# Optimization experiments

Hardware: AMD Instinct MI355X
Metric: run time of the kernel (lower is better)

Reference implementation:

```python
import jax, jax.numpy as jnp
import numpy as np

NUM_STEPS = 5


def setup_inputs() -> dict:
    key = jax.random.key(0)
    ks = jax.random.split(key, 12)
    B, N, H, E, A = 8, 1024, 64, 2, 8
    initial_state = jax.random.normal(ks[0], (B, N, H), dtype=jnp.float32)
    annotation = jax.random.normal(ks[1], (B, N, A), dtype=jnp.float32)
    # sparse-ish positive adjacency, scaled so matmul outputs don't saturate gates
    adj_matrix = jax.random.uniform(ks[2], (B, N, 2 * N * E), dtype=jnp.float32) * 0.01
    s = 0.05
    W_edge = jax.random.normal(ks[3], (H, H * E), dtype=jnp.float32) * s
    b_edge = jax.random.normal(ks[4], (H * E,), dtype=jnp.float32) * s
    W_gate = jax.random.normal(ks[5], (3 * H, H), dtype=jnp.float32) * s
    b_gate = jax.random.normal(ks[6], (H,), dtype=jnp.float32) * s
    W_hid = jax.random.normal(ks[7], (H + A, H), dtype=jnp.float32) * s
    b_hid = jax.random.normal(ks[8], (H,), dtype=jnp.float32) * s
    W_out = jax.random.normal(ks[9], (H, 1), dtype=jnp.float32) * s
    b_out = jax.random.normal(ks[10], (1,), dtype=jnp.float32) * s
    return dict(initial_state=initial_state, annotation=annotation, adj_matrix=adj_matrix,
                W_edge=W_edge, b_edge=b_edge, W_gate=W_gate, b_gate=b_gate,
                W_hid=W_hid, b_hid=b_hid, W_out=W_out, b_out=b_out)


def reference(initial_state, annotation, adj_matrix, W_edge, b_edge,
              W_gate, b_gate, W_hid, b_hid, W_out, b_out):
    B, N, H = initial_state.shape
    E = W_edge.shape[1] // H
    boundary = N * E
    A_in = adj_matrix[:, :, :boundary]   # [B, N, N*E]
    A_out = adj_matrix[:, :, boundary:]  # [B, N, N*E]

    h = initial_state
    for _ in range(NUM_STEPS):
        # Linear(H, H*E) then view/transpose to [B, N*E, H].
        # Original computes incoming_edge and outgoing_edge with the SAME
        # linear on the SAME input -> identical tensors; compute once.
        edge = jnp.einsum('bnh,he->bne', h, W_edge) + b_edge      # [B, N, H*E]
        edge = edge.reshape(B, N, H, E).transpose(0, 3, 1, 2).reshape(B, N * E, H)
        a_in = jnp.matmul(A_in, edge)    # [B, N, H]
        a_out = jnp.matmul(A_out, edge)  # [B, N, H]
        a = jnp.concatenate([a_in, a_out, h], axis=2)             # [B, N, 3H]
        # update and reset use the same gate linear -> equal; compute once.
        z = jax.nn.sigmoid(jnp.einsum('bnk,kh->bnh', a, W_gate) + b_gate)
        a_r = jnp.concatenate([a_in, a_out, z * h], axis=2)
        h_tilde = jnp.tanh(jnp.einsum('bnk,kh->bnh', a_r, W_gate) + b_gate)
        h = (1.0 - z) * h + z * h_tilde

    # task_id not in {18, 19}: node-level output head
    ha = jnp.concatenate([h, annotation], axis=2)                 # [B, N, H+A]
    out = jnp.tanh(jnp.einsum('bnk,kh->bnh', ha, W_hid) + b_hid)  # [B, N, H]
    out = (jnp.einsum('bnh,ho->bno', out, W_out) + b_out).sum(axis=2)  # [B, N]
    return out
```

## Files before the change

kernel.cpp:

```cpp
#include <hip/hip_runtime.h>
#include <math.h>

#define BN    8
#define NN    1024
#define HH    64
#define ADIM  8
#define STEPS 5
#define K2    2048
#define ROWS  (BN*NN)

typedef __attribute__((ext_vector_type(8))) short bf16x8;
typedef __attribute__((ext_vector_type(4))) float f32x4;

__device__ __forceinline__ unsigned short f2bf(float f) {
    unsigned int u = __float_as_uint(f);
    u += 0x7FFF + ((u >> 16) & 1);
    return (unsigned short)(u >> 16);
}
__device__ __forceinline__ float bf2f(unsigned short h) {
    return __uint_as_float(((unsigned int)h) << 16);
}

__global__ __launch_bounds__(256) void conv_adj(
    const float* __restrict__ in, unsigned short* __restrict__ out)
{
    int tid = blockIdx.x * 256 + threadIdx.x;
    #pragma unroll
    for (int i = 0; i < 4; ++i) {
        size_t idx = (size_t)tid + (size_t)i * 2097152;
        float4 v = ((const float4*)in)[idx];
        ushort4 o;
        o.x = f2bf(v.x); o.y = f2bf(v.y); o.z = f2bf(v.z); o.w = f2bf(v.w);
        ((ushort4*)out)[idx] = o;
    }
}

__global__ __launch_bounds__(256) void prep_pack(
    const float* __restrict__ Wg, const float* __restrict__ We,
    unsigned short* __restrict__ wgp, unsigned short* __restrict__ wep)
{
    int t = blockIdx.x * 256 + threadIdx.x;
    if (t < 12288) {
        int k = t >> 6, c = t & 63;
        float v = Wg[t];
        unsigned short hi = f2bf(v);
        unsigned short lo = f2bf(v - bf2f(hi));
        wgp[(size_t)c * 192 + k] = hi;
        wgp[(size_t)(64 + c) * 192 + k] = lo;
    } else if (t < 20480) {
        int u = t - 12288;
        int k = u >> 7, c = u & 127;
        float v = We[u];
        unsigned short hi = f2bf(v);
        unsigned short lo = f2bf(v - bf2f(hi));
        wep[(size_t)c * 64 + k] = hi;
        wep[(size_t)(128 + c) * 64 + k] = lo;
    }
}

__global__ __launch_bounds__(256) void init_kernel(
    const float* __restrict__ init_state,
    const float* __restrict__ We, const float* __restrict__ be,
    float* __restrict__ h_ws, unsigned short* __restrict__ edge_t)
{
    __shared__ float h_lds[4][65];
    int t = threadIdx.x;
    int r = t >> 6, hp = t & 63;
    int row = blockIdx.x * 4 + r;
    float hv = init_state[(size_t)row * 64 + hp];
    h_ws[(size_t)row * 64 + hp] = hv;
    h_lds[r][hp] = hv;
    __syncthreads();
    int b = row >> 10, n = row & 1023;
    #pragma unroll
    for (int e = 0; e < 2; ++e) {
        float acc = be[hp * 2 + e];
        #pragma unroll 8
        for (int c = 0; c < 64; ++c)
            acc += h_lds[r][c] * We[c * 128 + hp * 2 + e];
        edge_t[((size_t)b * 64 + hp) * K2 + e * NN + n] = f2bf(acc);
    }
}

__global__ __launch_bounds__(512) void step_kernel(
    const unsigned short* __restrict__ adjb,
    const unsigned short* __restrict__ ein,
    unsigned short* __restrict__ eout,
    float* __restrict__ h_ws,
    const unsigned short* __restrict__ wgp,
    const unsigned short* __restrict__ wep,
    const float* __restrict__ bg,
    const float* __restrict__ be,
    int do_edge)
{
    __shared__ __attribute__((aligned(16))) unsigned short Bs[2][64][264];
    __shared__ __attribute__((aligned(16))) unsigned short Xhi[32][200];
    __shared__ __attribute__((aligned(16))) unsigned short Xlo[32][200];
    __shared__ __attribute__((aligned(16))) float          hf [32][68];
    __shared__ __attribute__((aligned(16))) unsigned short HNhi[32][72];
    __shared__ __attribute__((aligned(16))) unsigned short HNlo[32][72];

    int t  = threadIdx.x;
    int b  = blockIdx.x >> 5;
    int mt = blockIdx.x & 31;
    int n0 = mt * 32;
    size_t hbase = ((size_t)(b * NN + n0)) * 64;

    {
        int r = t >> 4, cg = (t & 15) * 4;
        float4 v = *(const float4*)(h_ws + hbase + (size_t)r * 64 + cg);
        float vv[4] = {v.x, v.y, v.z, v.w};
        #pragma unroll
        for (int j = 0; j < 4; ++j) {
            float hv = vv[j];
            unsigned short hi = f2bf(hv), lo = f2bf(hv - bf2f(hi));
            Xhi[r][128 + cg + j] = hi;
            Xlo[r][128 + cg + j] = lo;
            hf[r][cg + j] = hv;
        }
    }

    int lane = t & 63, w = t >> 6, l15 = lane & 15, q = lane >> 4;
    int dir = w >> 2, rh = (w >> 1) & 1, kc = w & 1;

    const unsigned short* Abase = adjb
        + ((size_t)(b * NN + n0 + rh * 16 + l15)) * 4096 + dir * K2 + kc * 128;

    int srow[4], scol[4];
    const unsigned short* sptr[4];
    #pragma unroll
    for (int i = 0; i < 4; ++i) {
        int u = i * 512 + t;
        srow[i] = u >> 5; scol[i] = (u & 31) * 8;
        sptr[i] = ein + ((size_t)b * 64 + srow[i]) * K2 + scol[i];
    }
    #pragma unroll
    for (int i = 0; i < 4; ++i)
        *(uint4*)&Bs[0][srow[i]][scol[i]] = *(const uint4*)(sptr[i]);
    __syncthreads();

    f32x4 acc[4];
    #pragma unroll
    for (int ct = 0; ct < 4; ++ct) acc[ct] = (f32x4){0.f, 0.f, 0.f, 0.f};

    bf16x8 af[4];
    #pragma unroll
    for (int ks = 0; ks < 4; ++ks)
        af[ks] = *(const bf16x8*)(Abase + ks * 32 + q * 8);

    #pragma unroll
    for (int c = 0; c < 8; ++c) {
        int buf = c & 1;
        uint4 g[4];
        bf16x8 afn[4];
        if (c < 7) {
            #pragma unroll
            for (int i = 0; i < 4; ++i)
                g[i] = *(const uint4*)(sptr[i] + (c + 1) * 256);
            #pragma unroll
            for (int ks = 0; ks < 4; ++ks)
                afn[ks] = *(const bf16x8*)(Abase + (c + 1) * 256 + ks * 32 + q * 8);
        }
        #pragma unroll
        for (int ks = 0; ks < 4; ++ks) {
            #pragma unroll
            for (int ct = 0; ct < 4; ++ct) {
                bf16x8 bfr = *(const bf16x8*)&Bs[buf][ct * 16 + l15][kc * 128 + ks * 32 + q * 8];
                acc[ct] = __builtin_amdgcn_mfma_f32_16x16x32_bf16(af[ks], bfr, acc[ct], 0, 0, 0);
            }
        }
        if (c < 7) {
            #pragma unroll
            for (int i = 0; i < 4; ++i)
                *(uint4*)&Bs[buf ^ 1][srow[i]][scol[i]] = g[i];
            #pragma unroll
            for (int ks = 0; ks < 4; ++ks) af[ks] = afn[ks];
        }
        __syncthreads();
    }

    float (*red)[16][68] = (float (*)[16][68])(&Bs[0][0][0]);
    int gg = w >> 1;
    if (kc == 1) {
        #pragma unroll
        for (int ct = 0; ct < 4; ++ct)
            #pragma unroll
            for (int i = 0; i < 4; ++i)
                red[gg][q * 4 + i][ct * 16 + l15] = acc[ct][i];
    }
    __syncthreads();
    if (kc == 0) {
        #pragma unroll
        for (int ct = 0; ct < 4; ++ct)
            #pragma unroll
            for (int i = 0; i < 4; ++i) {
                float v = acc[ct][i] + red[gg][q * 4 + i][ct * 16 + l15];
                unsigned short hi = f2bf(v), lo = f2bf(v - bf2f(hi));
                int r  = rh * 16 + q * 4 + i;
                int cc = dir * 64 + ct * 16 + l15;
                Xhi[r][cc] = hi;
                Xlo[r][cc] = lo;
            }
    }
    __syncthreads();

    int mg = w & 1, cg16 = w >> 1;
    int arow = mg * 16 + l15;
    int cc = cg16 * 16 + l15;
    const unsigned short* wcol = wgp + (size_t)cc * 192;
    f32x4 as = (f32x4){0.f, 0.f, 0.f, 0.f}, az;

    #pragma unroll
    for (int ks = 0; ks < 4; ++ks) {
        bf16x8 ah = *(const bf16x8*)&Xhi[arow][ks * 32 + q * 8];
        bf16x8 al = *(const bf16x8*)&Xlo[arow][ks * 32 + q * 8];
        const unsigned short* wb = wcol + ks * 32 + q * 8;
        bf16x8 bh = *(const bf16x8*)wb;
        bf16x8 bl = *(const bf16x8*)(wb + 64 * 192);
        as = __builtin_amdgcn_mfma_f32_16x16x32_bf16(ah, bh, as, 0, 0, 0);
        as = __builtin_amdgcn_mfma_f32_16x16x32_bf16(ah, bl, as, 0, 0, 0);
        as = __builtin_amdgcn_mfma_f32_16x16x32_bf16(al, bh, as, 0, 0, 0);
    }
    az = as;
    #pragma unroll
    for (int ks = 4; ks < 6; ++ks) {
        bf16x8 ah = *(const bf16x8*)&Xhi[arow][ks * 32 + q * 8];
        bf16x8 al = *(const bf16x8*)&Xlo[arow][ks * 32 + q * 8];
        const unsigned short* wb = wcol + ks * 32 + q * 8;
        bf16x8 bh = *(const bf16x8*)wb;
        bf16x8 bl = *(const bf16x8*)(wb + 64 * 192);
        az = __builtin_amdgcn_mfma_f32_16x16x32_bf16(ah, bh, az, 0, 0, 0);
        az = __builtin_amdgcn_mfma_f32_16x16x32_bf16(ah, bl, az, 0, 0, 0);
        az = __builtin_amdgcn_mfma_f32_16x16x32_bf16(al, bh, az, 0, 0, 0);
    }
    __syncthreads();

    float zv[4], hv[4];
    float bgv = bg[cc];
    #pragma unroll
    for (int i = 0; i < 4; ++i) {
        int r = mg * 16 + q * 4 + i;
        float z = 1.f / (1.f + __expf(-(az[i] + bgv)));
        float h = hf[r][cc];
        zv[i] = z; hv[i] = h;
        float zh = z * h;
        unsigned short hi = f2bf(zh), lo = f2bf(zh - bf2f(hi));
        Xhi[r][128 + cc] = hi;
        Xlo[r][128 + cc] = lo;
    }
    __syncthreads();

    #pragma unroll
    for (int ks = 4; ks < 6; ++ks) {
        bf16x8 ah = *(const bf16x8*)&Xhi[arow][ks * 32 + q * 8];
        bf16x8 al = *(const bf16x8*)&Xlo[arow][ks * 32 + q * 8];
        const unsigned short* wb = wcol + ks * 32 + q * 8;
        bf16x8 bh = *(const bf16x8*)wb;
        bf16x8 bl = *(const bf16x8*)(wb + 64 * 192);
        as = __builtin_amdgcn_mfma_f32_16x16x32_bf16(ah, bh, as, 0, 0, 0);
        as = __builtin_amdgcn_mfma_f32_16x16x32_bf16(ah, bl, as, 0, 0, 0);
        as = __builtin_amdgcn_mfma_f32_16x16x32_bf16(al, bh, as, 0, 0, 0);
    }

    #pragma unroll
    for (int i = 0; i < 4; ++i) {
        int r = mg * 16 + q * 4 + i;
        float ht = tanhf(as[i] + bgv);
        float z  = zv[i];
        float hn = (1.f - z) * hv[i] + z * ht;
        h_ws[hbase + (size_t)r * 64 + cc] = hn;
        if (do_edge) {
            unsigned short hi = f2bf(hn), lo = f2bf(hn - bf2f(hi));
            HNhi[r][cc] = hi;
            HNlo[r][cc] = lo;
        }
    }
    if (!do_edge) return;
    __syncthreads();

    int me = w & 1, cb2 = (w >> 1) * 2;
    int erow = me * 16 + l15;
    f32x4 ae[2];
    ae[0] = ae[1] = (f32x4){0.f, 0.f, 0.f, 0.f};
    #pragma unroll
    for (int ks = 0; ks < 2; ++ks) {
        bf16x8 ah = *(const bf16x8*)&HNhi[erow][ks * 32 + q * 8];
        bf16x8 al = *(const bf16x8*)&HNlo[erow][ks * 32 + q * 8];
        #pragma unroll
        for (int p = 0; p < 2; ++p) {
            int ec = (cb2 + p) * 16 + l15;
            const unsigned short* wb = wep + (size_t)ec * 64 + ks * 32 + q * 8;
            bf16x8 bh = *(const bf16x8*)wb;
            bf16x8 bl = *(const bf16x8*)(wb + 128 * 64);
            ae[p] = __builtin_amdgcn_mfma_f32_16x16x32_bf16(ah, bh, ae[p], 0, 0, 0);
            ae[p] = __builtin_amdgcn_mfma_f32_16x16x32_bf16(ah, bl, ae[p], 0, 0, 0);
            ae[p] = __builtin_amdgcn_mfma_f32_16x16x32_bf16(al, bh, ae[p], 0, 0, 0);
        }
    }
    #pragma unroll
    for (int p = 0; p < 2; ++p) {
        int ec = (cb2 + p) * 16 + l15;
        float bev = be[ec];
        int hp2 = ec >> 1, e = ec & 1;
        size_t ebase = ((size_t)b * 64 + hp2) * K2 + (size_t)e * NN
                     + n0 + me * 16 + q * 4;
        ushort4 ev;
        ev.x = f2bf(ae[p][0] + bev);
        ev.y = f2bf(ae[p][1] + bev);
        ev.z = f2bf(ae[p][2] + bev);
        ev.w = f2bf(ae[p][3] + bev);
        *(ushort4*)(eout + ebase) = ev;
    }
}

__global__ __launch_bounds__(256) void head_kernel(
    const float* __restrict__ h_ws, const float* __restrict__ ann,
    const float* __restrict__ Wh, const float* __restrict__ bh,
    const float* __restrict__ Wo, const float* __restrict__ bo,
    float* __restrict__ out)
{
    __shared__ float Wh_l[72 * 64];
    __shared__ float ha[4][72];
    int t = threadIdx.x;
    #pragma unroll
    for (int l = 0; l < 18; ++l) {
        int idx = t + l * 256;
        Wh_l[idx] = Wh[idx];
    }
    int r = t >> 6, hp = t & 63;
    int row = blockIdx.x * 4 + r;
    ha[r][hp] = h_ws[(size_t)row * 64 + hp];
    if (hp < ADIM) ha[r][64 + hp] = ann[(size_t)row * ADIM + hp];
    __syncthreads();

    float acc = bh[hp];
    #pragma unroll 8
    for (int k = 0; k < 72; ++k)
        acc += ha[r][k] * Wh_l[k * 64 + hp];
    float v = tanhf(acc) * Wo[hp];
    #pragma unroll
    for (int o = 32; o; o >>= 1) v += __shfl_down(v, o, 64);
    if (hp == 0) out[row] = v + bo[0];
}

extern "C" void kernel_launch(void* const* d_in, const int* in_sizes, int n_in,
                              void* d_out, int out_size, void* d_ws, size_t ws_size,
                              hipStream_t stream) {
    const float* init_state = (const float*)d_in[0];
    const float* ann = (const float*)d_in[1];
    const float* adj = (const float*)d_in[2];
    const float* We  = (const float*)d_in[3];
    const float* be  = (const float*)d_in[4];
    const float* Wg  = (const float*)d_in[5];
    const float* bg  = (const float*)d_in[6];
    const float* Wh  = (const float*)d_in[7];
    const float* bh  = (const float*)d_in[8];
    const float* Wo  = (const float*)d_in[9];
    const float* bo  = (const float*)d_in[10];
    float* out = (float*)d_out;

    char* wsb = (char*)d_ws;
    unsigned short* adj_bf = (unsigned short*)wsb;
    unsigned short* edge_a = (unsigned short*)(wsb + 67108864);
    unsigned short* edge_b = (unsigned short*)(wsb + 69206016);
    float*          h_ws   = (float*)(wsb + 71303168);
    unsigned short* wgp    = (unsigned short*)(wsb + 73400320);
    unsigned short* wep    = (unsigned short*)(wsb + 73449472);

    conv_adj<<<dim3(8192), dim3(256), 0, stream>>>(adj, adj_bf);
    prep_pack<<<dim3(80), dim3(256), 0, stream>>>(Wg, We, wgp, wep);
    init_kernel<<<dim3(ROWS / 4), dim3(256), 0, stream>>>(init_state, We, be, h_ws, edge_a);
    for (int s = 0; s < STEPS; ++s) {
        const unsigned short* ein = (s & 1) ? edge_b : edge_a;
        unsigned short* eo        = (s & 1) ? edge_a : edge_b;
        step_kernel<<<dim3(256), dim3(512), 0, stream>>>(
            adj_bf, ein, eo, h_ws, wgp, wep, bg, be, (s < STEPS - 1) ? 1 : 0);
    }
    head_kernel<<<dim3(ROWS / 4), dim3(256), 0, stream>>>(h_ws, ann, Wh, bh, Wo, bo, out);
}
```

Measured before the change: 384.1 us.

## Pre-tile adjacency and edge buffers into MFMA fragment layout, drop LDS staging

The bf16 adjacency conversion now writes a tiled layout, and the edge tensor is stored in a matching tiled layout. Each MFMA fragment becomes one contiguous 16-byte load per lane straight from global memory. The step kernel's LDS double-buffered B staging, its barriers and its register prefetch pipeline are replaced by direct global loads in a simple unrolled loop. This removes LDS traffic and synchronisation, but load latency now has to be hidden by the unroll and by occupancy, and each B fragment is re-read from global or L2 by every wave.

```diff
diff --git a/kernel.cpp b/kernel.cpp
--- a/kernel.cpp
+++ b/kernel.cpp
@@ -21,17 +21,24 @@
     return __uint_as_float(((unsigned int)h) << 16);
 }
 
+
 __global__ __launch_bounds__(256) void conv_adj(
     const float* __restrict__ in, unsigned short* __restrict__ out)
 {
     int tid = blockIdx.x * 256 + threadIdx.x;
-    #pragma unroll
-    for (int i = 0; i < 4; ++i) {
-        size_t idx = (size_t)tid + (size_t)i * 2097152;
-        float4 v = ((const float4*)in)[idx];
+    int r   = tid >> 7;
+    int dkb = tid & 127;
+    int b = r >> 10, n = r & 1023;
+    int dir = dkb >> 6, kb = dkb & 63;
+    const float* src = in + ((size_t)r << 12) + (dkb << 5);
+    unsigned short* dst = out
+        + ((((((size_t)b * 2 + dir) * 64 + kb) * 64 + (n >> 4)) << 4) + (n & 15)) * 32;
+    #pragma unroll
+    for (int i = 0; i < 8; ++i) {
+        float4 v = ((const float4*)src)[i];
         ushort4 o;
         o.x = f2bf(v.x); o.y = f2bf(v.y); o.z = f2bf(v.z); o.w = f2bf(v.w);
-        ((ushort4*)out)[idx] = o;
+        ((ushort4*)dst)[i] = o;
     }
 }
 
@@ -58,6 +65,12 @@
     }
 }
 
+__device__ __forceinline__ size_t edge_addr(int b, int h, int k) {
+    int kb = k >> 5, hb = h >> 4;
+    return (((size_t)b * 64 + kb) * 4 + hb) * 512
+         + (size_t)(h & 15) * 32 + (k & 31);
+}
+
 __global__ __launch_bounds__(256) void init_kernel(
     const float* __restrict__ init_state,
     const float* __restrict__ We, const float* __restrict__ be,
@@ -78,12 +91,12 @@
         #pragma unroll 8
         for (int c = 0; c < 64; ++c)
             acc += h_lds[r][c] * We[c * 128 + hp * 2 + e];
-        edge_t[((size_t)b * 64 + hp) * K2 + e * NN + n] = f2bf(acc);
+        edge_t[edge_addr(b, hp, e * NN + n)] = f2bf(acc);
     }
 }
 
 __global__ __launch_bounds__(512) void step_kernel(
-    const unsigned short* __restrict__ adjb,
+    const unsigned short* __restrict__ adjf,
     const unsigned short* __restrict__ ein,
     unsigned short* __restrict__ eout,
     float* __restrict__ h_ws,
@@ -93,12 +106,12 @@
     const float* __restrict__ be,
     int do_edge)
 {
-    __shared__ __attribute__((aligned(16))) unsigned short Bs[2][64][264];
     __shared__ __attribute__((aligned(16))) unsigned short Xhi[32][200];
     __shared__ __attribute__((aligned(16))) unsigned short Xlo[32][200];
     __shared__ __attribute__((aligned(16))) float          hf [32][68];
     __shared__ __attribute__((aligned(16))) unsigned short HNhi[32][72];
     __shared__ __attribute__((aligned(16))) unsigned short HNlo[32][72];
+    __shared__ __attribute__((aligned(16))) float          red[4][16][68];
 
     int t  = threadIdx.x;
     int b  = blockIdx.x >> 5;
@@ -122,64 +135,28 @@
 
     int lane = t & 63, w = t >> 6, l15 = lane & 15, q = lane >> 4;
     int dir = w >> 2, rh = (w >> 1) & 1, kc = w & 1;
-
-    const unsigned short* Abase = adjb
-        + ((size_t)(b * NN + n0 + rh * 16 + l15)) * 4096 + dir * K2 + kc * 128;
-
-    int srow[4], scol[4];
-    const unsigned short* sptr[4];
-    #pragma unroll
-    for (int i = 0; i < 4; ++i) {
-        int u = i * 512 + t;
-        srow[i] = u >> 5; scol[i] = (u & 31) * 8;
-        sptr[i] = ein + ((size_t)b * 64 + srow[i]) * K2 + scol[i];
-    }
-    #pragma unroll
-    for (int i = 0; i < 4; ++i)
-        *(uint4*)&Bs[0][srow[i]][scol[i]] = *(const uint4*)(sptr[i]);
-    __syncthreads();
+    int nb  = mt * 2 + rh;
+    int loff = l15 * 32 + q * 8;
+
+    const unsigned short* Ap = adjf
+        + ((((size_t)(b * 2 + dir) * 64 + kc * 32) * 64 + nb) * 512) + loff;
+    const unsigned short* Bp = ein
+        + (((size_t)b * 64 + kc * 32) * 4) * 512 + loff;
 
     f32x4 acc[4];
     #pragma unroll
     for (int ct = 0; ct < 4; ++ct) acc[ct] = (f32x4){0.f, 0.f, 0.f, 0.f};
 
-    bf16x8 af[4];
-    #pragma unroll
-    for (int ks = 0; ks < 4; ++ks)
-        af[ks] = *(const bf16x8*)(Abase + ks * 32 + q * 8);
-
-    #pragma unroll
-    for (int c = 0; c < 8; ++c) {
-        int buf = c & 1;
-        uint4 g[4];
-        bf16x8 afn[4];
-        if (c < 7) {
-            #pragma unroll
-            for (int i = 0; i < 4; ++i)
-                g[i] = *(const uint4*)(sptr[i] + (c + 1) * 256);
-            #pragma unroll
-            for (int ks = 0; ks < 4; ++ks)
-                afn[ks] = *(const bf16x8*)(Abase + (c + 1) * 256 + ks * 32 + q * 8);
+    #pragma unroll 4
+    for (int kb = 0; kb < 32; ++kb) {
+        bf16x8 af = *(const bf16x8*)(Ap + kb * 32768);
+        #pragma unroll
+        for (int ct = 0; ct < 4; ++ct) {
+            bf16x8 bfr = *(const bf16x8*)(Bp + kb * 2048 + ct * 512);
+            acc[ct] = __builtin_amdgcn_mfma_f32_16x16x32_bf16(af, bfr, acc[ct], 0, 0, 0);
         }
-        #pragma unroll
-        for (int ks = 0; ks < 4; ++ks) {
-            #pragma unroll
-            for (int ct = 0; ct < 4; ++ct) {
-                bf16x8 bfr = *(const bf16x8*)&Bs[buf][ct * 16 + l15][kc * 128 + ks * 32 + q * 8];
-                acc[ct] = __builtin_amdgcn_mfma_f32_16x16x32_bf16(af[ks], bfr, acc[ct], 0, 0, 0);
-            }
-        }
-        if (c < 7) {
-            #pragma unroll
-            for (int i = 0; i < 4; ++i)
-                *(uint4*)&Bs[buf ^ 1][srow[i]][scol[i]] = g[i];
-            #pragma unroll
-            for (int ks = 0; ks < 4; ++ks) af[ks] = afn[ks];
-        }
-        __syncthreads();
-    }
-
-    float (*red)[16][68] = (float (*)[16][68])(&Bs[0][0][0]);
+    }
+
     int gg = w >> 1;
     if (kc == 1) {
         #pragma unroll
@@ -301,15 +278,14 @@
     for (int p = 0; p < 2; ++p) {
         int ec = (cb2 + p) * 16 + l15;
         float bev = be[ec];
-        int hp2 = ec >> 1, e = ec & 1;
-        size_t ebase = ((size_t)b * 64 + hp2) * K2 + (size_t)e * NN
-                     + n0 + me * 16 + q * 4;
+        int h = ec >> 1, e = ec & 1;
+        int k = e * NN + n0 + me * 16 + q * 4;
         ushort4 ev;
         ev.x = f2bf(ae[p][0] + bev);
         ev.y = f2bf(ae[p][1] + bev);
         ev.z = f2bf(ae[p][2] + bev);
         ev.w = f2bf(ae[p][3] + bev);
-        *(ushort4*)(eout + ebase) = ev;
+        *(ushort4*)(eout + edge_addr(b, h, k)) = ev;
     }
 }
 
@@ -360,21 +336,21 @@
     float* out = (float*)d_out;
 
     char* wsb = (char*)d_ws;
-    unsigned short* adj_bf = (unsigned short*)wsb;
+    unsigned short* adj_f  = (unsigned short*)wsb;
     unsigned short* edge_a = (unsigned short*)(wsb + 67108864);
     unsigned short* edge_b = (unsigned short*)(wsb + 69206016);
     float*          h_ws   = (float*)(wsb + 71303168);
     unsigned short* wgp    = (unsigned short*)(wsb + 73400320);
     unsigned short* wep    = (unsigned short*)(wsb + 73449472);
 
-    conv_adj<<<dim3(8192), dim3(256), 0, stream>>>(adj, adj_bf);
+    conv_adj<<<dim3(4096), dim3(256), 0, stream>>>(adj, adj_f);
     prep_pack<<<dim3(80), dim3(256), 0, stream>>>(Wg, We, wgp, wep);
     init_kernel<<<dim3(ROWS / 4), dim3(256), 0, stream>>>(init_state, We, be, h_ws, edge_a);
     for (int s = 0; s < STEPS; ++s) {
         const unsigned short* ein = (s & 1) ? edge_b : edge_a;
         unsigned short* eo        = (s & 1) ? edge_a : edge_b;
         step_kernel<<<dim3(256), dim3(512), 0, stream>>>(
-            adj_bf, ein, eo, h_ws, wgp, wep, bg, be, (s < STEPS - 1) ? 1 : 0);
+            adj_f, ein, eo, h_ws, wgp, wep, bg, be, (s < STEPS - 1) ? 1 : 0);
     }
     head_kernel<<<dim3(ROWS / 4), dim3(256), 0, stream>>>(h_ws, ann, Wh, bh, Wo, bo, out);
 }
```

Result: slower. 429.8 us (+11.9%).

## Fuse all stages into one cooperative persistent kernel with grid syncs

Applied to the files above, without the earlier changes.

Merges adjacency bf16 conversion, weight packing, initial edge projection, the five GGNN steps and the output head into a single cooperative kernel of 256 blocks. Steps are separated by grid.sync, and the hidden state stays in LDS across steps instead of going through global memory. This removes about eight kernel launches and the h round-trips through global memory. In exchange, the large adjacency conversion now runs on only 256 blocks, grid-wide barriers add cost, and the rows each block converts may not match the rows it later reads. The adjacency conversion is followed only by a grid sync, so later reads by other blocks rely on that barrier for ordering.

```diff
diff --git a/kernel.cpp b/kernel.cpp
--- a/kernel.cpp
+++ b/kernel.cpp
@@ -1,5 +1,8 @@
 #include <hip/hip_runtime.h>
+#include <hip/hip_cooperative_groups.h>
 #include <math.h>
+
+namespace cg = cooperative_groups;
 
 #define BN    8
 #define NN    1024
@@ -21,77 +24,20 @@
     return __uint_as_float(((unsigned int)h) << 16);
 }
 
-__global__ __launch_bounds__(256) void conv_adj(
-    const float* __restrict__ in, unsigned short* __restrict__ out)
-{
-    int tid = blockIdx.x * 256 + threadIdx.x;
-    #pragma unroll
-    for (int i = 0; i < 4; ++i) {
-        size_t idx = (size_t)tid + (size_t)i * 2097152;
-        float4 v = ((const float4*)in)[idx];
-        ushort4 o;
-        o.x = f2bf(v.x); o.y = f2bf(v.y); o.z = f2bf(v.z); o.w = f2bf(v.w);
-        ((ushort4*)out)[idx] = o;
-    }
-}
-
-__global__ __launch_bounds__(256) void prep_pack(
-    const float* __restrict__ Wg, const float* __restrict__ We,
-    unsigned short* __restrict__ wgp, unsigned short* __restrict__ wep)
-{
-    int t = blockIdx.x * 256 + threadIdx.x;
-    if (t < 12288) {
-        int k = t >> 6, c = t & 63;
-        float v = Wg[t];
-        unsigned short hi = f2bf(v);
-        unsigned short lo = f2bf(v - bf2f(hi));
-        wgp[(size_t)c * 192 + k] = hi;
-        wgp[(size_t)(64 + c) * 192 + k] = lo;
-    } else if (t < 20480) {
-        int u = t - 12288;
-        int k = u >> 7, c = u & 127;
-        float v = We[u];
-        unsigned short hi = f2bf(v);
-        unsigned short lo = f2bf(v - bf2f(hi));
-        wep[(size_t)c * 64 + k] = hi;
-        wep[(size_t)(128 + c) * 64 + k] = lo;
-    }
-}
-
-__global__ __launch_bounds__(256) void init_kernel(
+__global__ __launch_bounds__(512) void mega(
+    const float* __restrict__ adj,
     const float* __restrict__ init_state,
+    const float* __restrict__ ann,
     const float* __restrict__ We, const float* __restrict__ be,
-    float* __restrict__ h_ws, unsigned short* __restrict__ edge_t)
-{
-    __shared__ float h_lds[4][65];
-    int t = threadIdx.x;
-    int r = t >> 6, hp = t & 63;
-    int row = blockIdx.x * 4 + r;
-    float hv = init_state[(size_t)row * 64 + hp];
-    h_ws[(size_t)row * 64 + hp] = hv;
-    h_lds[r][hp] = hv;
-    __syncthreads();
-    int b = row >> 10, n = row & 1023;
-    #pragma unroll
-    for (int e = 0; e < 2; ++e) {
-        float acc = be[hp * 2 + e];
-        #pragma unroll 8
-        for (int c = 0; c < 64; ++c)
-            acc += h_lds[r][c] * We[c * 128 + hp * 2 + e];
-        edge_t[((size_t)b * 64 + hp) * K2 + e * NN + n] = f2bf(acc);
-    }
-}
-
-__global__ __launch_bounds__(512) void step_kernel(
-    const unsigned short* __restrict__ adjb,
-    const unsigned short* __restrict__ ein,
-    unsigned short* __restrict__ eout,
-    float* __restrict__ h_ws,
-    const unsigned short* __restrict__ wgp,
-    const unsigned short* __restrict__ wep,
-    const float* __restrict__ bg,
-    const float* __restrict__ be,
-    int do_edge)
+    const float* __restrict__ Wg, const float* __restrict__ bg,
+    const float* __restrict__ Wh, const float* __restrict__ bh,
+    const float* __restrict__ Wo, const float* __restrict__ bo,
+    unsigned short* __restrict__ adjb,
+    unsigned short* __restrict__ edge_a,
+    unsigned short* __restrict__ edge_b,
+    unsigned short* __restrict__ wgp,
+    unsigned short* __restrict__ wep,
+    float* __restrict__ out)
 {
     __shared__ __attribute__((aligned(16))) unsigned short Bs[2][64][264];
     __shared__ __attribute__((aligned(16))) unsigned short Xhi[32][200];
@@ -100,6 +46,8 @@
     __shared__ __attribute__((aligned(16))) unsigned short HNhi[32][72];
     __shared__ __attribute__((aligned(16))) unsigned short HNlo[32][72];
 
+    cg::grid_group grid = cg::this_grid();
+
     int t  = threadIdx.x;
     int b  = blockIdx.x >> 5;
     int mt = blockIdx.x & 31;
@@ -107,18 +55,65 @@
     size_t hbase = ((size_t)(b * NN + n0)) * 64;
 
     {
-        int r = t >> 4, cg = (t & 15) * 4;
-        float4 v = *(const float4*)(h_ws + hbase + (size_t)r * 64 + cg);
-        float vv[4] = {v.x, v.y, v.z, v.w};
-        #pragma unroll
-        for (int j = 0; j < 4; ++j) {
-            float hv = vv[j];
-            unsigned short hi = f2bf(hv), lo = f2bf(hv - bf2f(hi));
-            Xhi[r][128 + cg + j] = hi;
-            Xlo[r][128 + cg + j] = lo;
-            hf[r][cg + j] = hv;
-        }
-    }
+        int gtid = blockIdx.x * 512 + t;
+        const float4* src = (const float4*)adj;
+        ushort4* dst = (ushort4*)adjb;
+        #pragma unroll 8
+        for (int i = 0; i < 64; ++i) {
+            size_t idx = (size_t)gtid + (size_t)i * 131072;
+            float4 v = src[idx];
+            ushort4 o;
+            o.x = f2bf(v.x); o.y = f2bf(v.y); o.z = f2bf(v.z); o.w = f2bf(v.w);
+            dst[idx] = o;
+        }
+    }
+    if (blockIdx.x == 0) {
+        for (int idx = t; idx < 12288; idx += 512) {
+            int k = idx >> 6, c = idx & 63;
+            float v = Wg[idx];
+            unsigned short hi = f2bf(v), lo = f2bf(v - bf2f(hi));
+            wgp[(size_t)c * 192 + k] = hi;
+            wgp[(size_t)(64 + c) * 192 + k] = lo;
+        }
+    } else if (blockIdx.x == 1) {
+        for (int idx = t; idx < 8192; idx += 512) {
+            int k = idx >> 7, c = idx & 127;
+            float v = We[idx];
+            unsigned short hi = f2bf(v), lo = f2bf(v - bf2f(hi));
+            wep[(size_t)c * 64 + k] = hi;
+            wep[(size_t)(128 + c) * 64 + k] = lo;
+        }
+    }
+    {
+        int r = t >> 4, cg4 = (t & 15) * 4;
+        float4 v = *(const float4*)(init_state + hbase + (size_t)r * 64 + cg4);
+        hf[r][cg4 + 0] = v.x; hf[r][cg4 + 1] = v.y;
+        hf[r][cg4 + 2] = v.z; hf[r][cg4 + 3] = v.w;
+    }
+    __syncthreads();
+    {
+        int r2 = t >> 4, tq = t & 15;
+        int n = n0 + r2;
+        float acc[8];
+        #pragma unroll
+        for (int m = 0; m < 8; ++m) acc[m] = be[tq * 8 + m];
+        #pragma unroll 4
+        for (int c = 0; c < 64; ++c) {
+            float hv = hf[r2][c];
+            float4 w0 = *(const float4*)&We[c * 128 + tq * 8];
+            float4 w1 = *(const float4*)&We[c * 128 + tq * 8 + 4];
+            acc[0] += hv * w0.x; acc[1] += hv * w0.y; acc[2] += hv * w0.z; acc[3] += hv * w0.w;
+            acc[4] += hv * w1.x; acc[5] += hv * w1.y; acc[6] += hv * w1.z; acc[7] += hv * w1.w;
+        }
+        #pragma unroll
+        for (int m = 0; m < 8; ++m) {
+            int o = tq * 8 + m;
+            int hp = o >> 1, e = o & 1;
+            edge_a[((size_t)b * 64 + hp) * K2 + e * NN + n] = f2bf(acc[m]);
+        }
+    }
+    __threadfence();
+    grid.sync();
 
     int lane = t & 63, w = t >> 6, l15 = lane & 15, q = lane >> 4;
     int dir = w >> 2, rh = (w >> 1) & 1, kc = w & 1;
@@ -127,220 +122,244 @@
         + ((size_t)(b * NN + n0 + rh * 16 + l15)) * 4096 + dir * K2 + kc * 128;
 
     int srow[4], scol[4];
-    const unsigned short* sptr[4];
     #pragma unroll
     for (int i = 0; i < 4; ++i) {
         int u = i * 512 + t;
         srow[i] = u >> 5; scol[i] = (u & 31) * 8;
-        sptr[i] = ein + ((size_t)b * 64 + srow[i]) * K2 + scol[i];
-    }
-    #pragma unroll
-    for (int i = 0; i < 4; ++i)
-        *(uint4*)&Bs[0][srow[i]][scol[i]] = *(const uint4*)(sptr[i]);
+    }
+
+    const unsigned short* ein = edge_a;
+    unsigned short* eout = edge_b;
+
+    for (int s = 0; s < STEPS; ++s) {
+        {
+            int r = t >> 4, cg4 = (t & 15) * 4;
+            #pragma unroll
+            for (int j = 0; j < 4; ++j) {
+                float hv = hf[r][cg4 + j];
+                unsigned short hi = f2bf(hv), lo = f2bf(hv - bf2f(hi));
+                Xhi[r][128 + cg4 + j] = hi;
+                Xlo[r][128 + cg4 + j] = lo;
+            }
+        }
+        const unsigned short* sptr[4];
+        #pragma unroll
+        for (int i = 0; i < 4; ++i)
+            sptr[i] = ein + ((size_t)b * 64 + srow[i]) * K2 + scol[i];
+        #pragma unroll
+        for (int i = 0; i < 4; ++i)
+            *(uint4*)&Bs[0][srow[i]][scol[i]] = *(const uint4*)(sptr[i]);
+        __syncthreads();
+
+        f32x4 acc[4];
+        #pragma unroll
+        for (int ct = 0; ct < 4; ++ct) acc[ct] = (f32x4){0.f, 0.f, 0.f, 0.f};
+
+        bf16x8 af[4];
+        #pragma unroll
+        for (int ks = 0; ks < 4; ++ks)
+            af[ks] = *(const bf16x8*)(Abase + ks * 32 + q * 8);
+
+        #pragma unroll
+        for (int c = 0; c < 8; ++c) {
+            int buf = c & 1;
+            uint4 g[4];
+            bf16x8 afn[4];
+            if (c < 7) {
+                #pragma unroll
+                for (int i = 0; i < 4; ++i)
+                    g[i] = *(const uint4*)(sptr[i] + (c + 1) * 256);
+                #pragma unroll
+                for (int ks = 0; ks < 4; ++ks)
+                    afn[ks] = *(const bf16x8*)(Abase + (c + 1) * 256 + ks * 32 + q * 8);
+            }
+            #pragma unroll
+            for (int ks = 0; ks < 4; ++ks) {
+                #pragma unroll
+                for (int ct = 0; ct < 4; ++ct) {
+                    bf16x8 bfr = *(const bf16x8*)&Bs[buf][ct * 16 + l15][kc * 128 + ks * 32 + q * 8];
+                    acc[ct] = __builtin_amdgcn_mfma_f32_16x16x32_bf16(af[ks], bfr, acc[ct], 0, 0, 0);
+                }
+            }
+            if (c < 7) {
+                #pragma unroll
+                for (int i = 0; i < 4; ++i)
+                    *(uint4*)&Bs[buf ^ 1][srow[i]][scol[i]] = g[i];
+                #pragma unroll
+                for (int ks = 0; ks < 4; ++ks) af[ks] = afn[ks];
+            }
+            __syncthreads();
+        }
+
+        float (*red)[16][68] = (float (*)[16][68])(&Bs[0][0][0]);
+        int gg = w >> 1;
+        if (kc == 1) {
+            #pragma unroll
+            for (int ct = 0; ct < 4; ++ct)
+                #pragma unroll
+                for (int i = 0; i < 4; ++i)
+                    red[gg][q * 4 + i][ct * 16 + l15] = acc[ct][i];
+        }
+        __syncthreads();
+        if (kc == 0) {
+            #pragma unroll
+            for (int ct = 0; ct < 4; ++ct)
+                #pragma unroll
+                for (int i = 0; i < 4; ++i) {
+                    float v = acc[ct][i] + red[gg][q * 4 + i][ct * 16 + l15];
+                    unsigned short hi = f2bf(v), lo = f2bf(v - bf2f(hi));
+                    int r  = rh * 16 + q * 4 + i;
+                    int cc2 = dir * 64 + ct * 16 + l15;
+                    Xhi[r][cc2] = hi;
+                    Xlo[r][cc2] = lo;
+                }
+        }
+        __syncthreads();
+
+        int mg = w & 1, cg16 = w >> 1;
+        int arow = mg * 16 + l15;
+        int cc = cg16 * 16 + l15;
+        const unsigned short* wcol = wgp + (size_t)cc * 192;
+        f32x4 as = (f32x4){0.f, 0.f, 0.f, 0.f}, az;
+
+        #pragma unroll
+        for (int ks = 0; ks < 4; ++ks) {
+            bf16x8 ah = *(const bf16x8*)&Xhi[arow][ks * 32 + q * 8];
+            bf16x8 al = *(const bf16x8*)&Xlo[arow][ks * 32 + q * 8];
+            const unsigned short* wb = wcol + ks * 32 + q * 8;
+            bf16x8 bh = *(const bf16x8*)wb;
+            bf16x8 bl = *(const bf16x8*)(wb + 64 * 192);
+            as = __builtin_amdgcn_mfma_f32_16x16x32_bf16(ah, bh, as, 0, 0, 0);
+            as = __builtin_amdgcn_mfma_f32_16x16x32_bf16(ah, bl, as, 0, 0, 0);
+            as = __builtin_amdgcn_mfma_f32_16x16x32_bf16(al, bh, as, 0, 0, 0);
+        }
+        az = as;
+        #pragma unroll
+        for (int ks = 4; ks < 6; ++ks) {
+            bf16x8 ah = *(const bf16x8*)&Xhi[arow][ks * 32 + q * 8];
+            bf16x8 al = *(const bf16x8*)&Xlo[arow][ks * 32 + q * 8];
+            const unsigned short* wb = wcol + ks * 32 + q * 8;
+            bf16x8 bh = *(const bf16x8*)wb;
+            bf16x8 bl = *(const bf16x8*)(wb + 64 * 192);
+            az = __builtin_amdgcn_mfma_f32_16x16x32_bf16(ah, bh, az, 0, 0, 0);
+            az = __builtin_amdgcn_mfma_f32_16x16x32_bf16(ah, bl, az, 0, 0, 0);
+            az = __builtin_amdgcn_mfma_f32_16x16x32_bf16(al, bh, az, 0, 0, 0);
+        }
+        __syncthreads();
+
+        float zv[4], hv[4];
+        float bgv = bg[cc];
+        #pragma unroll
+        for (int i = 0; i < 4; ++i) {
+            int r = mg * 16 + q * 4 + i;
+            float z = 1.f / (1.f + __expf(-(az[i] + bgv)));
+            float h = hf[r][cc];
+            zv[i] = z; hv[i] = h;
+            float zh = z * h;
+            unsigned short hi = f2bf(zh), lo = f2bf(zh - bf2f(hi));
+            Xhi[r][128 + cc] = hi;
+            Xlo[r][128 + cc] = lo;
+        }
+        __syncthreads();
+
+        #pragma unroll
+        for (int ks = 4; ks < 6; ++ks) {
+            bf16x8 ah = *(const bf16x8*)&Xhi[arow][ks * 32 + q * 8];
+            bf16x8 al = *(const bf16x8*)&Xlo[arow][ks * 32 + q * 8];
+            const unsigned short* wb = wcol + ks * 32 + q * 8;
+            bf16x8 bh = *(const bf16x8*)wb;
+            bf16x8 bl = *(const bf16x8*)(wb + 64 * 192);
+            as = __builtin_amdgcn_mfma_f32_16x16x32_bf16(ah, bh, as, 0, 0, 0);
+            as = __builtin_amdgcn_mfma_f32_16x16x32_bf16(ah, bl, as, 0, 0, 0);
+            as = __builtin_amdgcn_mfma_f32_16x16x32_bf16(al, bh, as, 0, 0, 0);
+        }
+
+        #pragma unroll
+        for (int i = 0; i < 4; ++i) {
+            int r = mg * 16 + q * 4 + i;
+            float ht = tanhf(as[i] + bgv);
+            float z  = zv[i];
+            float hn = (1.f - z) * hv[i] + z * ht;
+            hf[r][cc] = hn;
+            if (s < STEPS - 1) {
+                unsigned short hi = f2bf(hn), lo = f2bf(hn - bf2f(hi));
+                HNhi[r][cc] = hi;
+                HNlo[r][cc] = lo;
+            }
+        }
+
+        if (s < STEPS - 1) {
+            __syncthreads();
+            int me = w & 1, cb2 = (w >> 1) * 2;
+            int erow = me * 16 + l15;
+            f32x4 ae[2];
+            ae[0] = ae[1] = (f32x4){0.f, 0.f, 0.f, 0.f};
+            #pragma unroll
+            for (int ks = 0; ks < 2; ++ks) {
+                bf16x8 ah = *(const bf16x8*)&HNhi[erow][ks * 32 + q * 8];
+                bf16x8 al = *(const bf16x8*)&HNlo[erow][ks * 32 + q * 8];
+                #pragma unroll
+                for (int p = 0; p < 2; ++p) {
+                    int ec = (cb2 + p) * 16 + l15;
+                    const unsigned short* wb = wep + (size_t)ec * 64 + ks * 32 + q * 8;
+                    bf16x8 bh = *(const bf16x8*)wb;
+                    bf16x8 bl = *(const bf16x8*)(wb + 128 * 64);
+                    ae[p] = __builtin_amdgcn_mfma_f32_16x16x32_bf16(ah, bh, ae[p], 0, 0, 0);
+                    ae[p] = __builtin_amdgcn_mfma_f32_16x16x32_bf16(ah, bl, ae[p], 0, 0, 0);
+                    ae[p] = __builtin_amdgcn_mfma_f32_16x16x32_bf16(al, bh, ae[p], 0, 0, 0);
+                }
+            }
+            #pragma unroll
+            for (int p = 0; p < 2; ++p) {
+                int ec = (cb2 + p) * 16 + l15;
+                float bev = be[ec];
+                int hp2 = ec >> 1, e = ec & 1;
+                size_t ebase = ((size_t)b * 64 + hp2) * K2 + (size_t)e * NN
+                             + n0 + me * 16 + q * 4;
+                ushort4 ev;
+                ev.x = f2bf(ae[p][0] + bev);
+                ev.y = f2bf(ae[p][1] + bev);
+                ev.z = f2bf(ae[p][2] + bev);
+                ev.w = f2bf(ae[p][3] + bev);
+                *(ushort4*)(eout + ebase) = ev;
+            }
+            __threadfence();
+            grid.sync();
+            const unsigned short* tmp = ein; ein = eout; eout = (unsigned short*)tmp;
+        }
+    }
+
     __syncthreads();
-
-    f32x4 acc[4];
-    #pragma unroll
-    for (int ct = 0; ct < 4; ++ct) acc[ct] = (f32x4){0.f, 0.f, 0.f, 0.f};
-
-    bf16x8 af[4];
-    #pragma unroll
-    for (int ks = 0; ks < 4; ++ks)
-        af[ks] = *(const bf16x8*)(Abase + ks * 32 + q * 8);
-
-    #pragma unroll
-    for (int c = 0; c < 8; ++c) {
-        int buf = c & 1;
-        uint4 g[4];
-        bf16x8 afn[4];
-        if (c < 7) {
-            #pragma unroll
-            for (int i = 0; i < 4; ++i)
-                g[i] = *(const uint4*)(sptr[i] + (c + 1) * 256);
-            #pragma unroll
-            for (int ks = 0; ks < 4; ++ks)
-                afn[ks] = *(const bf16x8*)(Abase + (c + 1) * 256 + ks * 32 + q * 8);
-        }
-        #pragma unroll
-        for (int ks = 0; ks < 4; ++ks) {
-            #pragma unroll
-            for (int ct = 0; ct < 4; ++ct) {
-                bf16x8 bfr = *(const bf16x8*)&Bs[buf][ct * 16 + l15][kc * 128 + ks * 32 + q * 8];
-                acc[ct] = __builtin_amdgcn_mfma_f32_16x16x32_bf16(af[ks], bfr, acc[ct], 0, 0, 0);
-            }
-        }
-        if (c < 7) {
-            #pragma unroll
-            for (int i = 0; i < 4; ++i)
-                *(uint4*)&Bs[buf ^ 1][srow[i]][scol[i]] = g[i];
-            #pragma unroll
-            for (int ks = 0; ks < 4; ++ks) af[ks] = afn[ks];
-        }
-        __syncthreads();
-    }
-
-    float (*red)[16][68] = (float (*)[16][68])(&Bs[0][0][0]);
-    int gg = w >> 1;
-    if (kc == 1) {
-        #pragma unroll
-        for (int ct = 0; ct < 4; ++ct)
-            #pragma unroll
-            for (int i = 0; i < 4; ++i)
-                red[gg][q * 4 + i][ct * 16 + l15] = acc[ct][i];
-    }
-    __syncthreads();
-    if (kc == 0) {
-        #pragma unroll
-        for (int ct = 0; ct < 4; ++ct)
-            #pragma unroll
-            for (int i = 0; i < 4; ++i) {
-                float v = acc[ct][i] + red[gg][q * 4 + i][ct * 16 + l15];
-                unsigned short hi = f2bf(v), lo = f2bf(v - bf2f(hi));
-                int r  = rh * 16 + q * 4 + i;
-                int cc = dir * 64 + ct * 16 + l15;
-                Xhi[r][cc] = hi;
-                Xlo[r][cc] = lo;
-            }
-    }
-    __syncthreads();
-
-    int mg = w & 1, cg16 = w >> 1;
-    int arow = mg * 16 + l15;
-    int cc = cg16 * 16 + l15;
-    const unsigned short* wcol = wgp + (size_t)cc * 192;
-    f32x4 as = (f32x4){0.f, 0.f, 0.f, 0.f}, az;
-
-    #pragma unroll
-    for (int ks = 0; ks < 4; ++ks) {
-        bf16x8 ah = *(const bf16x8*)&Xhi[arow][ks * 32 + q * 8];
-        bf16x8 al = *(const bf16x8*)&Xlo[arow][ks * 32 + q * 8];
-        const unsigned short* wb = wcol + ks * 32 + q * 8;
-        bf16x8 bh = *(const bf16x8*)wb;
-        bf16x8 bl = *(const bf16x8*)(wb + 64 * 192);
-        as = __builtin_amdgcn_mfma_f32_16x16x32_bf16(ah, bh, as, 0, 0, 0);
-        as = __builtin_amdgcn_mfma_f32_16x16x32_bf16(ah, bl, as, 0, 0, 0);
-        as = __builtin_amdgcn_mfma_f32_16x16x32_bf16(al, bh, as, 0, 0, 0);
-    }
-    az = as;
-    #pragma unroll
-    for (int ks = 4; ks < 6; ++ks) {
-        bf16x8 ah = *(const bf16x8*)&Xhi[arow][ks * 32 + q * 8];
-        bf16x8 al = *(const bf16x8*)&Xlo[arow][ks * 32 + q * 8];
-        const unsigned short* wb = wcol + ks * 32 + q * 8;
-        bf16x8 bh = *(const bf16x8*)wb;
-        bf16x8 bl = *(const bf16x8*)(wb + 64 * 192);
-        az = __builtin_amdgcn_mfma_f32_16x16x32_bf16(ah, bh, az, 0, 0, 0);
-        az = __builtin_amdgcn_mfma_f32_16x16x32_bf16(ah, bl, az, 0, 0, 0);
-        az = __builtin_amdgcn_mfma_f32_16x16x32_bf16(al, bh, az, 0, 0, 0);
-    }
-    __syncthreads();
-
-    float zv[4], hv[4];
-    float bgv = bg[cc];
-    #pragma unroll
-    for (int i = 0; i < 4; ++i) {
-        int r = mg * 16 + q * 4 + i;
-        float z = 1.f / (1.f + __expf(-(az[i] + bgv)));
-        float h = hf[r][cc];
-        zv[i] = z; hv[i] = h;
-        float zh = z * h;
-        unsigned short hi = f2bf(zh), lo = f2bf(zh - bf2f(hi));
-        Xhi[r][128 + cc] = hi;
-        Xlo[r][128 + cc] = lo;
-    }
-    __syncthreads();
-
-    #pragma unroll
-    for (int ks = 4; ks < 6; ++ks) {
-        bf16x8 ah = *(const bf16x8*)&Xhi[arow][ks * 32 + q * 8];
-        bf16x8 al = *(const bf16x8*)&Xlo[arow][ks * 32 + q * 8];
-        const unsigned short* wb = wcol + ks * 32 + q * 8;
-        bf16x8 bh = *(const bf16x8*)wb;
-        bf16x8 bl = *(const bf16x8*)(wb + 64 * 192);
-        as = __builtin_amdgcn_mfma_f32_16x16x32_bf16(ah, bh, as, 0, 0, 0);
-        as = __builtin_amdgcn_mfma_f32_16x16x32_bf16(ah, bl, as, 0, 0, 0);
-        as = __builtin_amdgcn_mfma_f32_16x16x32_bf16(al, bh, as, 0, 0, 0);
-    }
-
-    #pragma unroll
-    for (int i = 0; i < 4; ++i) {
-        int r = mg * 16 + q * 4 + i;
-        float ht = tanhf(as[i] + bgv);
-        float z  = zv[i];
-        float hn = (1.f - z) * hv[i] + z * ht;
-        h_ws[hbase + (size_t)r * 64 + cc] = hn;
-        if (do_edge) {
-            unsigned short hi = f2bf(hn), lo = f2bf(hn - bf2f(hi));
-            HNhi[r][cc] = hi;
-            HNlo[r][cc] = lo;
-        }
-    }
-    if (!do_edge) return;
-    __syncthreads();
-
-    int me = w & 1, cb2 = (w >> 1) * 2;
-    int erow = me * 16 + l15;
-    f32x4 ae[2];
-    ae[0] = ae[1] = (f32x4){0.f, 0.f, 0.f, 0.f};
-    #pragma unroll
-    for (int ks = 0; ks < 2; ++ks) {
-        bf16x8 ah = *(const bf16x8*)&HNhi[erow][ks * 32 + q * 8];
-        bf16x8 al = *(const bf16x8*)&HNlo[erow][ks * 32 + q * 8];
-        #pragma unroll
-        for (int p = 0; p < 2; ++p) {
-            int ec = (cb2 + p) * 16 + l15;
-            const unsigned short* wb = wep + (size_t)ec * 64 + ks * 32 + q * 8;
-            bf16x8 bh = *(const bf16x8*)wb;
-            bf16x8 bl = *(const bf16x8*)(wb + 128 * 64);
-            ae[p] = __builtin_amdgcn_mfma_f32_16x16x32_bf16(ah, bh, ae[p], 0, 0, 0);
-            ae[p] = __builtin_amdgcn_mfma_f32_16x16x32_bf16(ah, bl, ae[p], 0, 0, 0);
-            ae[p] = __builtin_amdgcn_mfma_f32_16x16x32_bf16(al, bh, ae[p], 0, 0, 0);
-        }
-    }
-    #pragma unroll
-    for (int p = 0; p < 2; ++p) {
-        int ec = (cb2 + p) * 16 + l15;
-        float bev = be[ec];
-        int hp2 = ec >> 1, e = ec & 1;
-        size_t ebase = ((size_t)b * 64 + hp2) * K2 + (size_t)e * NN
-                     + n0 + me * 16 + q * 4;
-        ushort4 ev;
-        ev.x = f2bf(ae[p][0] + bev);
-        ev.y = f2bf(ae[p][1] + bev);
-        ev.z = f2bf(ae[p][2] + bev);
-        ev.w = f2bf(ae[p][3] + bev);
-        *(ushort4*)(eout + ebase) = ev;
-    }
-}
-
-__global__ __launch_bounds__(256) void head_kernel(
-    const float* __restrict__ h_ws, const float* __restrict__ ann,
-    const float* __restrict__ Wh, const float* __restrict__ bh,
-    const float* __restrict__ Wo, const float* __restrict__ bo,
-    float* __restrict__ out)
-{
-    __shared__ float Wh_l[72 * 64];
-    __shared__ float ha[4][72];
-    int t = threadIdx.x;
-    #pragma unroll
-    for (int l = 0; l < 18; ++l) {
-        int idx = t + l * 256;
-        Wh_l[idx] = Wh[idx];
-    }
-    int r = t >> 6, hp = t & 63;
-    int row = blockIdx.x * 4 + r;
-    ha[r][hp] = h_ws[(size_t)row * 64 + hp];
-    if (hp < ADIM) ha[r][64 + hp] = ann[(size_t)row * ADIM + hp];
-    __syncthreads();
-
-    float acc = bh[hp];
-    #pragma unroll 8
-    for (int k = 0; k < 72; ++k)
-        acc += ha[r][k] * Wh_l[k * 64 + hp];
-    float v = tanhf(acc) * Wo[hp];
-    #pragma unroll
-    for (int o = 32; o; o >>= 1) v += __shfl_down(v, o, 64);
-    if (hp == 0) out[row] = v + bo[0];
+    {
+        int r = t >> 4, hq = (t & 15) * 4;
+        int row = b * NN + n0 + r;
+        float av[ADIM];
+        #pragma unroll
+        for (int j = 0; j < ADIM; ++j) av[j] = ann[(size_t)row * ADIM + j];
+        float acc[4];
+        #pragma unroll
+        for (int i = 0; i < 4; ++i) acc[i] = bh[hq + i];
+        #pragma unroll 8
+        for (int k = 0; k < 64; ++k) {
+            float hv = hf[r][k];
+            float4 wv = *(const float4*)&Wh[k * 64 + hq];
+            acc[0] += hv * wv.x; acc[1] += hv * wv.y;
+            acc[2] += hv * wv.z; acc[3] += hv * wv.w;
+        }
+        #pragma unroll
+        for (int k = 0; k < ADIM; ++k) {
+            float4 wv = *(const float4*)&Wh[(64 + k) * 64 + hq];
+            acc[0] += av[k] * wv.x; acc[1] += av[k] * wv.y;
+            acc[2] += av[k] * wv.z; acc[3] += av[k] * wv.w;
+        }
+        float v = 0.f;
+        #pragma unroll
+        for (int i = 0; i < 4; ++i)
+            v += tanhf(acc[i]) * Wo[hq + i];
+        #pragma unroll
+        for (int m = 8; m; m >>= 1) v += __shfl_xor(v, m, 64);
+        if ((t & 15) == 0) out[row] = v + bo[0];
+    }
 }
 
 extern "C" void kernel_launch(void* const* d_in, const int* in_sizes, int n_in,
@@ -360,21 +379,19 @@
     float* out = (float*)d_out;
 
     char* wsb = (char*)d_ws;
-    unsigned short* adj_bf = (unsigned short*)wsb;
+    unsigned short* adjb   = (unsigned short*)wsb;
     unsigned short* edge_a = (unsigned short*)(wsb + 67108864);
     unsigned short* edge_b = (unsigned short*)(wsb + 69206016);
-    float*          h_ws   = (float*)(wsb + 71303168);
-    unsigned short* wgp    = (unsigned short*)(wsb + 73400320);
-    unsigned short* wep    = (unsigned short*)(wsb + 73449472);
-
-    conv_adj<<<dim3(8192), dim3(256), 0, stream>>>(adj, adj_bf);
-    prep_pack<<<dim3(80), dim3(256), 0, stream>>>(Wg, We, wgp, wep);
-    init_kernel<<<dim3(ROWS / 4), dim3(256), 0, stream>>>(init_state, We, be, h_ws, edge_a);
-    for (int s = 0; s < STEPS; ++s) {
-        const unsigned short* ein = (s & 1) ? edge_b : edge_a;
-        unsigned short* eo        = (s & 1) ? edge_a : edge_b;
-        step_kernel<<<dim3(256), dim3(512), 0, stream>>>(
-            adj_bf, ein, eo, h_ws, wgp, wep, bg, be, (s < STEPS - 1) ? 1 : 0);
-    }
-    head_kernel<<<dim3(ROWS / 4), dim3(256), 0, stream>>>(h_ws, ann, Wh, bh, Wo, bo, out);
+    unsigned short* wgp    = (unsigned short*)(wsb + 71303168);
+    unsigned short* wep    = (unsigned short*)(wsb + 71352320);
+
+    void* args[] = {
+        (void*)&adj, (void*)&init_state, (void*)&ann,
+        (void*)&We, (void*)&be, (void*)&Wg, (void*)&bg,
+        (void*)&Wh, (void*)&bh, (void*)&Wo, (void*)&bo,
+        (void*)&adjb, (void*)&edge_a, (void*)&edge_b,
+        (void*)&wgp, (void*)&wep, (void*)&out
+    };
+    hipLaunchCooperativeKernel((const void*)mega, dim3(256), dim3(512),
+                               args, 0, stream);
 }
```

Result: slower. 829.2 us (+115.9%).
